# Optimization experiments

Hardware: AMD Instinct MI355X
Metric: run time of the kernel (lower is better)

The kernel has to match this reference:

```python
import jax, jax.numpy as jnp
import numpy as np
import math

SCALED = True
SUBSEQUENT_MASK = True
B, SQ, SK, D, DV = 8, 2048, 2048, 1024, 1024


def _build_mask(query_lens, key_lens, sq, sk, causal):
    # (B, Sq, Sk) boolean validity mask: rows >= q_len and cols >= k_len are masked.
    qm = jnp.arange(sq)[None, :, None] < query_lens[:, None, None]
    km = jnp.arange(sk)[None, None, :] < key_lens[:, None, None]
    mask = qm & km
    if causal:
        mask = mask & (jnp.arange(sk)[None, None, :] <= jnp.arange(sq)[None, :, None])
    return mask


def _masked_softmax(scores, mask):
    # Stable masked softmax; fully-masked rows yield exactly 0 (matches the
    # original's NaN -> 0 replacement) without producing NaNs.
    neg = jnp.finfo(scores.dtype).min
    s = jnp.where(mask, scores, neg)
    m = jnp.max(s, axis=-1, keepdims=True)
    e = jnp.where(mask, jnp.exp(s - m), jnp.zeros((), scores.dtype))
    denom = jnp.sum(e, axis=-1, keepdims=True)
    return e / jnp.where(denom == 0, jnp.ones((), scores.dtype), denom)


def setup_inputs() -> dict:
    key = jax.random.key(0)
    kq, kk, kv, kql, kkl = jax.random.split(key, 5)
    return {
        "queries": jax.random.normal(kq, (B, SQ, D), dtype=jnp.float32),
        "keys": jax.random.normal(kk, (B, SK, D), dtype=jnp.float32),
        "values": jax.random.normal(kv, (B, SK, DV), dtype=jnp.float32),
        "query_lens": jax.random.randint(kql, (B,), 1, SQ + 1),
        "key_lens": jax.random.randint(kkl, (B,), 1, SK + 1),
    }


def reference(queries, keys, values, query_lens, key_lens):
    # scores: (B, Sq, Sk)
    scores = jnp.einsum("bqd,bkd->bqk", queries, keys)
    if SCALED:
        scores = scores / math.sqrt(queries.shape[2])
    mask = _build_mask(query_lens, key_lens, queries.shape[1], keys.shape[1], SUBSEQUENT_MASK)
    weights = _masked_softmax(scores, mask)
    context = jnp.einsum("bqk,bkv->bqv", weights, values)
    return (context, weights)
```

## Files before the change

kernel.cpp:

```cpp
#include <hip/hip_runtime.h>
#include <hip/hip_bf16.h>

#define B_   8
#define SQ_  2048
#define SK_  2048
#define D_   1024
#define DV_  1024

typedef __bf16 bf16;
typedef __attribute__((ext_vector_type(4))) __bf16 bf16x4;
typedef __attribute__((ext_vector_type(8))) __bf16 bf16x8;
typedef __attribute__((ext_vector_type(4))) float  f32x4;

__global__ __launch_bounds__(512, 4)
void scores_kernel(const float* __restrict__ Q, const float* __restrict__ K,
                   const int* __restrict__ qlens, const int* __restrict__ klens,
                   float* __restrict__ Wout)
{
    const int b  = blockIdx.z;
    const int q0 = blockIdx.y * 128;
    const int k0 = blockIdx.x * 128;
    if (k0 > q0 + 127) return;
    const int qlen = qlens[b], klen = klens[b];
    if (q0 >= qlen || k0 >= klen) return;

    __shared__ __align__(16) bf16 Qs[2][128][72];
    __shared__ __align__(16) bf16 Ks[2][128][72];

    const int tid  = threadIdx.x;
    const int lane = tid & 63;
    const int w    = tid >> 6;
    const int wq   = w >> 1, wk = w & 1;

    const float* Qb = Q + (size_t)b * SQ_ * D_;
    const float* Kb = K + (size_t)b * SK_ * D_;

    float4 qreg[4], kreg[4];
    int srow[4], sc4[4];
    #pragma unroll
    for (int i = 0; i < 4; ++i) {
        int s = tid + i * 512;
        srow[i] = s >> 4;
        sc4[i]  = (s & 15) << 2;
    }

    auto load_tile = [&](int d0) {
        #pragma unroll
        for (int i = 0; i < 4; ++i) {
            qreg[i] = *(const float4*)(Qb + (size_t)(q0 + srow[i]) * D_ + d0 + sc4[i]);
            kreg[i] = *(const float4*)(Kb + (size_t)(k0 + srow[i]) * D_ + d0 + sc4[i]);
        }
    };
    auto store_tile = [&](int buf) {
        #pragma unroll
        for (int i = 0; i < 4; ++i) {
            bf16x4 qb = { (bf16)qreg[i].x, (bf16)qreg[i].y, (bf16)qreg[i].z, (bf16)qreg[i].w };
            bf16x4 kb = { (bf16)kreg[i].x, (bf16)kreg[i].y, (bf16)kreg[i].z, (bf16)kreg[i].w };
            *(bf16x4*)&Qs[buf][srow[i]][sc4[i]] = qb;
            *(bf16x4*)&Ks[buf][srow[i]][sc4[i]] = kb;
        }
    };

    f32x4 acc[2][4] = {};

    load_tile(0);
    store_tile(0);
    __syncthreads();

    for (int it = 0; it < 16; ++it) {
        const int cur = it & 1;
        if (it < 15) load_tile((it + 1) * 64);
        #pragma unroll
        for (int kk = 0; kk < 2; ++kk) {
            const int koff = kk * 32 + ((lane >> 4) << 3);
            bf16x8 a[2], bb[4];
            #pragma unroll
            for (int m = 0; m < 2; ++m)
                a[m] = *(const bf16x8*)&Qs[cur][32 * wq + 16 * m + (lane & 15)][koff];
            #pragma unroll
            for (int n = 0; n < 4; ++n)
                bb[n] = *(const bf16x8*)&Ks[cur][64 * wk + 16 * n + (lane & 15)][koff];
            #pragma unroll
            for (int m = 0; m < 2; ++m)
                #pragma unroll
                for (int n = 0; n < 4; ++n)
                    acc[m][n] = __builtin_amdgcn_mfma_f32_16x16x32_bf16(a[m], bb[n], acc[m][n], 0, 0, 0);
        }
        if (it < 15) store_tile(1 - cur);
        __syncthreads();
    }

    float* Wb = Wout + (size_t)b * SQ_ * SK_;
    const int rb = q0 + 32 * wq + ((lane >> 4) << 2);
    const int cb = k0 + 64 * wk + (lane & 15);
    #pragma unroll
    for (int m = 0; m < 2; ++m)
        #pragma unroll
        for (int n = 0; n < 4; ++n)
            #pragma unroll
            for (int r = 0; r < 4; ++r)
                Wb[(size_t)(rb + 16 * m + r) * SK_ + (cb + 16 * n)] = acc[m][n][r] * 0.03125f;
}

__global__ __launch_bounds__(256)
void softmax_kernel(const int* __restrict__ qlens, const int* __restrict__ klens,
                    float* __restrict__ W)
{
    const int bq = blockIdx.x;
    const int b  = bq >> 11;
    const int q  = bq & 2047;
    const int qlen = qlens[b], klen = klens[b];
    int kmax = 0;
    if (q < qlen) kmax = min(klen, q + 1);

    float4* row = (float4*)(W + (size_t)bq * SK_);
    const int tid = threadIdx.x;

    float4 x[2];
    float m = -INFINITY;
    #pragma unroll
    for (int i = 0; i < 2; ++i) {
        int v4 = tid + i * 256;
        int kb = v4 << 2;
        if (kb < kmax) x[i] = row[v4];
        else           x[i] = make_float4(-INFINITY, -INFINITY, -INFINITY, -INFINITY);
        float* xe = (float*)&x[i];
        #pragma unroll
        for (int e = 0; e < 4; ++e) {
            if (kb + e >= kmax) xe[e] = -INFINITY;
            m = fmaxf(m, xe[e]);
        }
    }
    #pragma unroll
    for (int off = 32; off > 0; off >>= 1) m = fmaxf(m, __shfl_xor(m, off, 64));
    __shared__ float red[4];
    if ((tid & 63) == 0) red[tid >> 6] = m;
    __syncthreads();
    m = fmaxf(fmaxf(red[0], red[1]), fmaxf(red[2], red[3]));
    __syncthreads();

    float sum = 0.f;
    #pragma unroll
    for (int i = 0; i < 2; ++i) {
        float* xe = (float*)&x[i];
        #pragma unroll
        for (int e = 0; e < 4; ++e) {
            float ev = (xe[e] == -INFINITY) ? 0.f : __expf(xe[e] - m);
            xe[e] = ev;
            sum += ev;
        }
    }
    #pragma unroll
    for (int off = 32; off > 0; off >>= 1) sum += __shfl_xor(sum, off, 64);
    if ((tid & 63) == 0) red[tid >> 6] = sum;
    __syncthreads();
    sum = red[0] + red[1] + red[2] + red[3];

    const float inv = (sum > 0.f) ? (1.f / sum) : 0.f;
    #pragma unroll
    for (int i = 0; i < 2; ++i) {
        float* xe = (float*)&x[i];
        float4 o = { xe[0] * inv, xe[1] * inv, xe[2] * inv, xe[3] * inv };
        row[tid + i * 256] = o;
    }
}

__global__ __launch_bounds__(512, 4)
void context_kernel(const float* __restrict__ W, const float* __restrict__ V,
                    const int* __restrict__ klens, float* __restrict__ Out)
{
    const int b  = blockIdx.z;
    const int q0 = blockIdx.y * 128;
    const int n0 = blockIdx.x * 128;
    const int klen = klens[b];
    const int kend = min(q0 + 128, (klen + 63) & ~63);
    const int nk   = kend >> 6;

    __shared__ __align__(16) bf16 Ws[2][128][72];
    __shared__ __align__(16) bf16 Vs[2][128][72];

    const int tid  = threadIdx.x;
    const int lane = tid & 63;
    const int w    = tid >> 6;
    const int wq   = w >> 1, wn = w & 1;

    const float* Wb = W + (size_t)b * SQ_ * SK_;
    const float* Vb = V + (size_t)b * SK_ * DV_;

    float4 wreg[4];
    float  vreg[2][8];
    int srow[4], sc4[4], vn[2], voct[2];
    #pragma unroll
    for (int i = 0; i < 4; ++i) {
        int s = tid + i * 512;
        srow[i] = s >> 4;
        sc4[i]  = (s & 15) << 2;
    }
    #pragma unroll
    for (int i = 0; i < 2; ++i) {
        int t = tid + i * 512;
        vn[i]   = t & 127;
        voct[i] = t >> 7;
    }

    auto load_tile = [&](int kk0) {
        #pragma unroll
        for (int i = 0; i < 4; ++i)
            wreg[i] = *(const float4*)(Wb + (size_t)(q0 + srow[i]) * SK_ + kk0 + sc4[i]);
        #pragma unroll
        for (int i = 0; i < 2; ++i)
            #pragma unroll
            for (int j = 0; j < 8; ++j)
                vreg[i][j] = Vb[(size_t)(kk0 + voct[i] * 8 + j) * DV_ + n0 + vn[i]];
    };
    auto store_tile = [&](int buf) {
        #pragma unroll
        for (int i = 0; i < 4; ++i) {
            bf16x4 wb = { (bf16)wreg[i].x, (bf16)wreg[i].y, (bf16)wreg[i].z, (bf16)wreg[i].w };
            *(bf16x4*)&Ws[buf][srow[i]][sc4[i]] = wb;
        }
        #pragma unroll
        for (int i = 0; i < 2; ++i) {
            bf16x8 vb = { (bf16)vreg[i][0], (bf16)vreg[i][1], (bf16)vreg[i][2], (bf16)vreg[i][3],
                          (bf16)vreg[i][4], (bf16)vreg[i][5], (bf16)vreg[i][6], (bf16)vreg[i][7] };
            *(bf16x8*)&Vs[buf][vn[i]][voct[i] * 8] = vb;
        }
    };

    f32x4 acc[2][4] = {};

    load_tile(0);
    store_tile(0);
    __syncthreads();

    for (int it = 0; it < nk; ++it) {
        const int cur = it & 1;
        if (it + 1 < nk) load_tile((it + 1) * 64);
        #pragma unroll
        for (int kk = 0; kk < 2; ++kk) {
            const int koff = kk * 32 + ((lane >> 4) << 3);
            bf16x8 a[2], bb[4];
            #pragma unroll
            for (int m = 0; m < 2; ++m)
                a[m] = *(const bf16x8*)&Ws[cur][32 * wq + 16 * m + (lane & 15)][koff];
            #pragma unroll
            for (int n = 0; n < 4; ++n)
                bb[n] = *(const bf16x8*)&Vs[cur][64 * wn + 16 * n + (lane & 15)][koff];
            #pragma unroll
            for (int m = 0; m < 2; ++m)
                #pragma unroll
                for (int n = 0; n < 4; ++n)
                    acc[m][n] = __builtin_amdgcn_mfma_f32_16x16x32_bf16(a[m], bb[n], acc[m][n], 0, 0, 0);
        }
        if (it + 1 < nk) store_tile(1 - cur);
        __syncthreads();
    }

    float* Ob = Out + (size_t)b * SQ_ * DV_;
    const int rb = q0 + 32 * wq + ((lane >> 4) << 2);
    const int cb = n0 + 64 * wn + (lane & 15);
    #pragma unroll
    for (int m = 0; m < 2; ++m)
        #pragma unroll
        for (int n = 0; n < 4; ++n)
            #pragma unroll
            for (int r = 0; r < 4; ++r)
                Ob[(size_t)(rb + 16 * m + r) * DV_ + (cb + 16 * n)] = acc[m][n][r];
}

extern "C" void kernel_launch(void* const* d_in, const int* in_sizes, int n_in,
                              void* d_out, int out_size, void* d_ws, size_t ws_size,
                              hipStream_t stream) {
    (void)in_sizes; (void)n_in; (void)out_size; (void)d_ws; (void)ws_size;
    const float* Q     = (const float*)d_in[0];
    const float* K     = (const float*)d_in[1];
    const float* V     = (const float*)d_in[2];
    const int*   qlens = (const int*)d_in[3];
    const int*   klens = (const int*)d_in[4];

    float* ctx = (float*)d_out;
    float* wts = ctx + (size_t)B_ * SQ_ * DV_;

    dim3 g1(SK_ / 128, SQ_ / 128, B_);
    scores_kernel<<<g1, 512, 0, stream>>>(Q, K, qlens, klens, wts);

    softmax_kernel<<<dim3(B_ * SQ_), 256, 0, stream>>>(qlens, klens, wts);

    dim3 g3(DV_ / 128, SQ_ / 128, B_);
    context_kernel<<<g3, 512, 0, stream>>>(wts, V, klens, ctx);
}
```

Baseline: 469.3 us.

## Pre-convert Q/K/V to bf16 and stage tiles via direct global-to-LDS loads

New measurement: 492.8 us. 1.05x slower.

```diff
diff --git a/kernel.cpp b/kernel.cpp
--- a/kernel.cpp
+++ b/kernel.cpp
@@ -12,10 +12,64 @@
 typedef __attribute__((ext_vector_type(8))) __bf16 bf16x8;
 typedef __attribute__((ext_vector_type(4))) float  f32x4;
 
+typedef const __attribute__((address_space(1))) void* gptr1;
+typedef __attribute__((address_space(3))) void*       lptr3;
+
+__device__ __forceinline__ void gload16(const void* g, void* l) {
+    __builtin_amdgcn_global_load_lds((gptr1)g, (lptr3)l, 16, 0, 0);
+}
+
+__global__ __launch_bounds__(256)
+void convert_kernel(const float* __restrict__ A, const float* __restrict__ Bm,
+                    bf16* __restrict__ dA, bf16* __restrict__ dB)
+{
+    const float* src = blockIdx.y ? Bm : A;
+    bf16*        dst = blockIdx.y ? dB : dA;
+    size_t i = ((size_t)blockIdx.x * 256 + threadIdx.x) * 8;
+    float4 v0 = *(const float4*)(src + i);
+    float4 v1 = *(const float4*)(src + i + 4);
+    bf16x8 o = { (bf16)v0.x, (bf16)v0.y, (bf16)v0.z, (bf16)v0.w,
+                 (bf16)v1.x, (bf16)v1.y, (bf16)v1.z, (bf16)v1.w };
+    *(bf16x8*)(dst + i) = o;
+}
+
+__global__ __launch_bounds__(256)
+void convVT_kernel(const float* __restrict__ V, bf16* __restrict__ VT)
+{
+    const int b  = blockIdx.z;
+    const int k0 = blockIdx.x * 64;
+    const int n0 = blockIdx.y * 64;
+    __shared__ bf16 T[64][72];
+
+    const int tid = threadIdx.x;
+    #pragma unroll
+    for (int i = 0; i < 4; ++i) {
+        int s  = tid + i * 256;
+        int r  = s >> 4;
+        int c4 = (s & 15) << 2;
+        float4 v = *(const float4*)(V + ((size_t)b * SK_ + (k0 + r)) * DV_ + n0 + c4);
+        T[r][c4 + 0] = (bf16)v.x;
+        T[r][c4 + 1] = (bf16)v.y;
+        T[r][c4 + 2] = (bf16)v.z;
+        T[r][c4 + 3] = (bf16)v.w;
+    }
+    __syncthreads();
+    #pragma unroll
+    for (int i = 0; i < 2; ++i) {
+        int s  = tid + i * 256;
+        int n  = s >> 3;
+        int c8 = (s & 7) << 3;
+        bf16x8 o;
+        #pragma unroll
+        for (int j = 0; j < 8; ++j) o[j] = T[c8 + j][n];
+        *(bf16x8*)(VT + ((size_t)b * DV_ + (n0 + n)) * SK_ + k0 + c8) = o;
+    }
+}
+
 __global__ __launch_bounds__(512, 4)
-void scores_kernel(const float* __restrict__ Q, const float* __restrict__ K,
-                   const int* __restrict__ qlens, const int* __restrict__ klens,
-                   float* __restrict__ Wout)
+void scores_bf_kernel(const bf16* __restrict__ Qbf, const bf16* __restrict__ Kbf,
+                      const int* __restrict__ qlens, const int* __restrict__ klens,
+                      float* __restrict__ Wout)
 {
     const int b  = blockIdx.z;
     const int q0 = blockIdx.y * 128;
@@ -24,52 +78,35 @@
     const int qlen = qlens[b], klen = klens[b];
     if (q0 >= qlen || k0 >= klen) return;
 
-    __shared__ __align__(16) bf16 Qs[2][128][72];
-    __shared__ __align__(16) bf16 Ks[2][128][72];
+    __shared__ __align__(16) bf16 Qs[2][128][64];
+    __shared__ __align__(16) bf16 Ks[2][128][64];
 
     const int tid  = threadIdx.x;
     const int lane = tid & 63;
     const int w    = tid >> 6;
     const int wq   = w >> 1, wk = w & 1;
 
-    const float* Qb = Q + (size_t)b * SQ_ * D_;
-    const float* Kb = K + (size_t)b * SK_ * D_;
-
-    float4 qreg[4], kreg[4];
-    int srow[4], sc4[4];
-    #pragma unroll
-    for (int i = 0; i < 4; ++i) {
-        int s = tid + i * 512;
-        srow[i] = s >> 4;
-        sc4[i]  = (s & 15) << 2;
-    }
-
-    auto load_tile = [&](int d0) {
-        #pragma unroll
-        for (int i = 0; i < 4; ++i) {
-            qreg[i] = *(const float4*)(Qb + (size_t)(q0 + srow[i]) * D_ + d0 + sc4[i]);
-            kreg[i] = *(const float4*)(Kb + (size_t)(k0 + srow[i]) * D_ + d0 + sc4[i]);
-        }
+    const bf16* Qb = Qbf + (size_t)b * SQ_ * D_ + (size_t)q0 * D_;
+    const bf16* Kb = Kbf + (size_t)b * SK_ * D_ + (size_t)k0 * D_;
+
+    const int r0 = tid >> 3;
+    const int c0 = (tid & 7) << 3;
+
+    auto stage = [&](int buf, int d0) {
+        gload16(Qb + (size_t)r0 * D_ + d0 + c0,        &Qs[buf][r0][c0]);
+        gload16(Qb + (size_t)(r0 + 64) * D_ + d0 + c0, &Qs[buf][r0 + 64][c0]);
+        gload16(Kb + (size_t)r0 * D_ + d0 + c0,        &Ks[buf][r0][c0]);
+        gload16(Kb + (size_t)(r0 + 64) * D_ + d0 + c0, &Ks[buf][r0 + 64][c0]);
     };
-    auto store_tile = [&](int buf) {
-        #pragma unroll
-        for (int i = 0; i < 4; ++i) {
-            bf16x4 qb = { (bf16)qreg[i].x, (bf16)qreg[i].y, (bf16)qreg[i].z, (bf16)qreg[i].w };
-            bf16x4 kb = { (bf16)kreg[i].x, (bf16)kreg[i].y, (bf16)kreg[i].z, (bf16)kreg[i].w };
-            *(bf16x4*)&Qs[buf][srow[i]][sc4[i]] = qb;
-            *(bf16x4*)&Ks[buf][srow[i]][sc4[i]] = kb;
-        }
-    };
 
     f32x4 acc[2][4] = {};
 
-    load_tile(0);
-    store_tile(0);
+    stage(0, 0);
     __syncthreads();
 
     for (int it = 0; it < 16; ++it) {
         const int cur = it & 1;
-        if (it < 15) load_tile((it + 1) * 64);
+        if (it < 15) stage(cur ^ 1, (it + 1) * 64);
         #pragma unroll
         for (int kk = 0; kk < 2; ++kk) {
             const int koff = kk * 32 + ((lane >> 4) << 3);
@@ -86,7 +123,6 @@
                 for (int n = 0; n < 4; ++n)
                     acc[m][n] = __builtin_amdgcn_mfma_f32_16x16x32_bf16(a[m], bb[n], acc[m][n], 0, 0, 0);
         }
-        if (it < 15) store_tile(1 - cur);
         __syncthreads();
     }
 
@@ -104,7 +140,7 @@
 
 __global__ __launch_bounds__(256)
 void softmax_kernel(const int* __restrict__ qlens, const int* __restrict__ klens,
-                    float* __restrict__ W)
+                    float* __restrict__ W, bf16* __restrict__ Wbf)
 {
     const int bq = blockIdx.x;
     const int b  = bq >> 11;
@@ -162,7 +198,186 @@
         float* xe = (float*)&x[i];
         float4 o = { xe[0] * inv, xe[1] * inv, xe[2] * inv, xe[3] * inv };
         row[tid + i * 256] = o;
-    }
+        if (Wbf) {
+            bf16x4 ob = { (bf16)o.x, (bf16)o.y, (bf16)o.z, (bf16)o.w };
+            *(bf16x4*)(Wbf + (size_t)bq * SK_ + ((size_t)(tid + i * 256) << 2)) = ob;
+        }
+    }
+}
+
+__global__ __launch_bounds__(512, 4)
+void context_bf_kernel(const bf16* __restrict__ Wbf, const bf16* __restrict__ VT,
+                       const int* __restrict__ qlens, const int* __restrict__ klens,
+                       float* __restrict__ Out)
+{
+    const int b  = blockIdx.z;
+    const int q0 = blockIdx.y * 128;
+    const int n0 = blockIdx.x * 128;
+    const int tid  = threadIdx.x;
+    const int qlen = qlens[b];
+
+    float* Ob = Out + (size_t)b * SQ_ * DV_;
+    if (q0 >= qlen) {
+        float4 z = make_float4(0.f, 0.f, 0.f, 0.f);
+        #pragma unroll
+        for (int i = 0; i < 8; ++i) {
+            int s  = tid + i * 512;
+            int r  = s >> 5;
+            int c4 = (s & 31) << 2;
+            *(float4*)(Ob + (size_t)(q0 + r) * DV_ + n0 + c4) = z;
+        }
+        return;
+    }
+
+    const int klen = klens[b];
+    const int kend = min(q0 + 128, (klen + 63) & ~63);
+    const int nk   = kend >> 6;
+
+    __shared__ __align__(16) bf16 Ws[2][128][64];
+    __shared__ __align__(16) bf16 Vs[2][128][64];
+
+    const int lane = tid & 63;
+    const int w    = tid >> 6;
+    const int wq   = w >> 1, wn = w & 1;
+
+    const bf16* Wb = Wbf + (size_t)b * SQ_ * SK_ + (size_t)q0 * SK_;
+    const bf16* Vb = VT  + (size_t)b * DV_ * SK_ + (size_t)n0 * SK_;
+
+    const int r0 = tid >> 3;
+    const int c0 = (tid & 7) << 3;
+
+    auto stage = [&](int buf, int kk0) {
+        gload16(Wb + (size_t)r0 * SK_ + kk0 + c0,        &Ws[buf][r0][c0]);
+        gload16(Wb + (size_t)(r0 + 64) * SK_ + kk0 + c0, &Ws[buf][r0 + 64][c0]);
+        gload16(Vb + (size_t)r0 * SK_ + kk0 + c0,        &Vs[buf][r0][c0]);
+        gload16(Vb + (size_t)(r0 + 64) * SK_ + kk0 + c0, &Vs[buf][r0 + 64][c0]);
+    };
+
+    f32x4 acc[2][4] = {};
+
+    stage(0, 0);
+    __syncthreads();
+
+    for (int it = 0; it < nk; ++it) {
+        const int cur = it & 1;
+        if (it + 1 < nk) stage(cur ^ 1, (it + 1) * 64);
+        #pragma unroll
+        for (int kk = 0; kk < 2; ++kk) {
+            const int koff = kk * 32 + ((lane >> 4) << 3);
+            bf16x8 a[2], bb[4];
+            #pragma unroll
+            for (int m = 0; m < 2; ++m)
+                a[m] = *(const bf16x8*)&Ws[cur][32 * wq + 16 * m + (lane & 15)][koff];
+            #pragma unroll
+            for (int n = 0; n < 4; ++n)
+                bb[n] = *(const bf16x8*)&Vs[cur][64 * wn + 16 * n + (lane & 15)][koff];
+            #pragma unroll
+            for (int m = 0; m < 2; ++m)
+                #pragma unroll
+                for (int n = 0; n < 4; ++n)
+                    acc[m][n] = __builtin_amdgcn_mfma_f32_16x16x32_bf16(a[m], bb[n], acc[m][n], 0, 0, 0);
+        }
+        __syncthreads();
+    }
+
+    const int rb = q0 + 32 * wq + ((lane >> 4) << 2);
+    const int cb = n0 + 64 * wn + (lane & 15);
+    #pragma unroll
+    for (int m = 0; m < 2; ++m)
+        #pragma unroll
+        for (int n = 0; n < 4; ++n)
+            #pragma unroll
+            for (int r = 0; r < 4; ++r)
+                Ob[(size_t)(rb + 16 * m + r) * DV_ + (cb + 16 * n)] = acc[m][n][r];
+}
+
+__global__ __launch_bounds__(512, 4)
+void scores_kernel(const float* __restrict__ Q, const float* __restrict__ K,
+                   const int* __restrict__ qlens, const int* __restrict__ klens,
+                   float* __restrict__ Wout)
+{
+    const int b  = blockIdx.z;
+    const int q0 = blockIdx.y * 128;
+    const int k0 = blockIdx.x * 128;
+    if (k0 > q0 + 127) return;
+    const int qlen = qlens[b], klen = klens[b];
+    if (q0 >= qlen || k0 >= klen) return;
+
+    __shared__ __align__(16) bf16 Qs[2][128][72];
+    __shared__ __align__(16) bf16 Ks[2][128][72];
+
+    const int tid  = threadIdx.x;
+    const int lane = tid & 63;
+    const int w    = tid >> 6;
+    const int wq   = w >> 1, wk = w & 1;
+
+    const float* Qb = Q + (size_t)b * SQ_ * D_;
+    const float* Kb = K + (size_t)b * SK_ * D_;
+
+    float4 qreg[4], kreg[4];
+    int srow[4], sc4[4];
+    #pragma unroll
+    for (int i = 0; i < 4; ++i) {
+        int s = tid + i * 512;
+        srow[i] = s >> 4;
+        sc4[i]  = (s & 15) << 2;
+    }
+
+    auto load_tile = [&](int d0) {
+        #pragma unroll
+        for (int i = 0; i < 4; ++i) {
+            qreg[i] = *(const float4*)(Qb + (size_t)(q0 + srow[i]) * D_ + d0 + sc4[i]);
+            kreg[i] = *(const float4*)(Kb + (size_t)(k0 + srow[i]) * D_ + d0 + sc4[i]);
+        }
+    };
+    auto store_tile = [&](int buf) {
+        #pragma unroll
+        for (int i = 0; i < 4; ++i) {
+            bf16x4 qb = { (bf16)qreg[i].x, (bf16)qreg[i].y, (bf16)qreg[i].z, (bf16)qreg[i].w };
+            bf16x4 kb = { (bf16)kreg[i].x, (bf16)kreg[i].y, (bf16)kreg[i].z, (bf16)kreg[i].w };
+            *(bf16x4*)&Qs[buf][srow[i]][sc4[i]] = qb;
+            *(bf16x4*)&Ks[buf][srow[i]][sc4[i]] = kb;
+        }
+    };
+
+    f32x4 acc[2][4] = {};
+    load_tile(0);
+    store_tile(0);
+    __syncthreads();
+
+    for (int it = 0; it < 16; ++it) {
+        const int cur = it & 1;
+        if (it < 15) load_tile((it + 1) * 64);
+        #pragma unroll
+        for (int kk = 0; kk < 2; ++kk) {
+            const int koff = kk * 32 + ((lane >> 4) << 3);
+            bf16x8 a[2], bb[4];
+            #pragma unroll
+            for (int m = 0; m < 2; ++m)
+                a[m] = *(const bf16x8*)&Qs[cur][32 * wq + 16 * m + (lane & 15)][koff];
+            #pragma unroll
+            for (int n = 0; n < 4; ++n)
+                bb[n] = *(const bf16x8*)&Ks[cur][64 * wk + 16 * n + (lane & 15)][koff];
+            #pragma unroll
+            for (int m = 0; m < 2; ++m)
+                #pragma unroll
+                for (int n = 0; n < 4; ++n)
+                    acc[m][n] = __builtin_amdgcn_mfma_f32_16x16x32_bf16(a[m], bb[n], acc[m][n], 0, 0, 0);
+        }
+        if (it < 15) store_tile(1 - cur);
+        __syncthreads();
+    }
+
+    float* Wb = Wout + (size_t)b * SQ_ * SK_;
+    const int rb = q0 + 32 * wq + ((lane >> 4) << 2);
+    const int cb = k0 + 64 * wk + (lane & 15);
+    #pragma unroll
+    for (int m = 0; m < 2; ++m)
+        #pragma unroll
+        for (int n = 0; n < 4; ++n)
+            #pragma unroll
+            for (int r = 0; r < 4; ++r)
+                Wb[(size_t)(rb + 16 * m + r) * SK_ + (cb + 16 * n)] = acc[m][n][r] * 0.03125f;
 }
 
 __global__ __launch_bounds__(512, 4)
@@ -228,7 +443,6 @@
     };
 
     f32x4 acc[2][4] = {};
-
     load_tile(0);
     store_tile(0);
     __syncthreads();
@@ -271,7 +485,7 @@
 extern "C" void kernel_launch(void* const* d_in, const int* in_sizes, int n_in,
                               void* d_out, int out_size, void* d_ws, size_t ws_size,
                               hipStream_t stream) {
-    (void)in_sizes; (void)n_in; (void)out_size; (void)d_ws; (void)ws_size;
+    (void)in_sizes; (void)n_in; (void)out_size;
     const float* Q     = (const float*)d_in[0];
     const float* K     = (const float*)d_in[1];
     const float* V     = (const float*)d_in[2];
@@ -281,11 +495,35 @@
     float* ctx = (float*)d_out;
     float* wts = ctx + (size_t)B_ * SQ_ * DV_;
 
-    dim3 g1(SK_ / 128, SQ_ / 128, B_);
-    scores_kernel<<<g1, 512, 0, stream>>>(Q, K, qlens, klens, wts);
-
-    softmax_kernel<<<dim3(B_ * SQ_), 256, 0, stream>>>(qlens, klens, wts);
-
-    dim3 g3(DV_ / 128, SQ_ / 128, B_);
-    context_kernel<<<g3, 512, 0, stream>>>(wts, V, klens, ctx);
-}
+    const size_t nQ = (size_t)B_ * SQ_ * D_;
+    const size_t nK = (size_t)B_ * SK_ * D_;
+    const size_t nV = (size_t)B_ * SK_ * DV_;
+    const size_t nW = (size_t)B_ * SQ_ * SK_;
+    const size_t ws_need = (nQ + nK + nV + nW) * sizeof(bf16);
+
+    if (d_ws && ws_size >= ws_need) {
+        bf16* qbf = (bf16*)d_ws;
+        bf16* kbf = qbf + nQ;
+        bf16* vbt = kbf + nK;
+        bf16* wbf = vbt + nV;
+
+        convert_kernel<<<dim3((unsigned)(nQ / (256 * 8)), 2), 256, 0, stream>>>(Q, K, qbf, kbf);
+        convVT_kernel<<<dim3(SK_ / 64, DV_ / 64, B_), 256, 0, stream>>>(V, vbt);
+
+        dim3 g1(SK_ / 128, SQ_ / 128, B_);
+        scores_bf_kernel<<<g1, 512, 0, stream>>>(qbf, kbf, qlens, klens, wts);
+
+        softmax_kernel<<<dim3(B_ * SQ_), 256, 0, stream>>>(qlens, klens, wts, wbf);
+
+        dim3 g3(DV_ / 128, SQ_ / 128, B_);
+        context_bf_kernel<<<g3, 512, 0, stream>>>(wbf, vbt, qlens, klens, ctx);
+    } else {
+        dim3 g1(SK_ / 128, SQ_ / 128, B_);
+        scores_kernel<<<g1, 512, 0, stream>>>(Q, K, qlens, klens, wts);
+
+        softmax_kernel<<<dim3(B_ * SQ_), 256, 0, stream>>>(qlens, klens, wts, (bf16*)nullptr);
+
+        dim3 g3(DV_ / 128, SQ_ / 128, B_);
+        context_kernel<<<g3, 512, 0, stream>>>(wts, V, klens, ctx);
+    }
+}
```
